# Performance work log

Hardware: AMD Instinct MI355X
Metric: run time of the kernel (lower is better)

## Reference

```python
import jax, jax.numpy as jnp
import numpy as np

B, NB, L, K, C, H = 4, 256, 64, 65, 512, 8
HD = C // H
SCALE = HD ** -0.5


def setup_inputs() -> dict:
    key = jax.random.key(0)
    k = jax.random.split(key, 6)
    x = jax.random.normal(k[0], (B, NB * L, C), dtype=jnp.float32)
    mask = jax.random.bernoulli(k[1], 0.3, (NB, L, K))
    d = jnp.arange(L)
    mask = mask.at[:, d, d].set(True)      # self edges always on
    mask = mask.at[:, :, L].set(True)      # block-node column always on
    edge_feats = jax.random.normal(k[2], (NB, L, K, 4), dtype=jnp.float32)
    qkv_w = jax.random.normal(k[3], (C, 3 * C), dtype=jnp.float32) * (C ** -0.5)
    qkv_b = jnp.zeros((3 * C,), dtype=jnp.float32)
    proj_w = jax.random.normal(k[4], (C, C), dtype=jnp.float32) * (C ** -0.5)
    proj_b = jnp.zeros((C,), dtype=jnp.float32)
    return {"x": x, "attn_mask": mask, "edge_feats": edge_feats,
            "qkv_w": qkv_w, "qkv_b": qkv_b, "proj_w": proj_w, "proj_b": proj_b}


def reference(x, attn_mask, edge_feats, qkv_w, qkv_b, proj_w, proj_b):
    # x: (B, N, C) with N = NB*L (no padding needed); pool = 1, layout LxL+1
    x_blk = x.reshape(B, NB, L, C)                       # query tokens per leaf block
    block_node = x_blk.mean(axis=2, keepdims=True)       # (B, NB, 1, C)
    kv = jnp.concatenate([x_blk, block_node], axis=2)    # (B, NB, K, C), K = L+1

    qkv_q = x_blk @ qkv_w + qkv_b
    qkv_kv = kv @ qkv_w + qkv_b
    q = qkv_q[..., :C].reshape(B, NB, L, H, HD)
    k = qkv_kv[..., C:2 * C].reshape(B, NB, K, H, HD)
    v = qkv_kv[..., 2 * C:].reshape(B, NB, K, H, HD)

    scores = jnp.einsum('bnqhd,bnkhd->bnqkh', q, k) * SCALE  # (B,NB,L,K,H)

    # physics bias: edge_feats[..., :4] broadcast over batch; special/diagonal overrides
    bp = jnp.broadcast_to(edge_feats[None, ..., :4], (B, NB, L, K, 4))
    bp = bp.at[:, :, :, L, :].set(0.0)
    bp = bp.at[:, :, :, L, 3].set(1.0)                    # block-node key column
    d = jnp.arange(L)
    bp = bp.at[:, :, d, d, :].set(0.0)
    bp = bp.at[:, :, d, d, 3].set(1.0)                    # self edge
    scores = scores + bp[..., 3:4]                        # channel 3 additive bias (all heads)

    mask = attn_mask[None, :, :, :, None]                 # (1,NB,L,K,1)
    scores = jnp.where(mask, scores, jnp.float32(-1e9))
    attn = jax.nn.softmax(scores, axis=3)

    out = jnp.einsum('bnqkh,bnkhd->bnqhd', attn, v).reshape(B, NB * L, C)
    return out @ proj_w + proj_b
```

## Files before the change

kernel.cpp:

```cpp
#include <hip/hip_runtime.h>
#include <hip/hip_bf16.h>
#include <math.h>

typedef unsigned short u16;
typedef __attribute__((ext_vector_type(8))) short s16x8;
typedef __attribute__((ext_vector_type(4))) float f32x4;

#define NB_ 256
#define L_  64
#define KK_ 65
#define C_  512
#define H_  8
#define NEDGE (256*64*65)
#define MTOT  65536

__device__ __forceinline__ float b2f(u16 u){
  union { unsigned int i; float f; } x; x.i = ((unsigned int)u) << 16; return x.f;
}
__device__ __forceinline__ u16 f2b(float f){
  union { float f; unsigned int i; } x; x.f = f;
  return (u16)((x.i + 0x7FFFu + ((x.i >> 16) & 1u)) >> 16);
}

__device__ __forceinline__ void gload_lds16(const u16* g, u16* l){
  __builtin_amdgcn_global_load_lds(
      (const __attribute__((address_space(1))) unsigned int*)g,
      (__attribute__((address_space(3))) unsigned int*)l,
      16, 0, 0);
}

__global__ void detect_dtype_kernel(const u16* __restrict__ x, int* __restrict__ flagdt){
  __shared__ int cnt;
  if (threadIdx.x == 0) cnt = 0;
  __syncthreads();
  u16 v = x[(size_t)threadIdx.x * 2 * 1001];
  int e = (v >> 7) & 0xFF;
  if (e >= 141) atomicAdd(&cnt, 1);
  __syncthreads();
  if (threadIdx.x == 0) *flagdt = (cnt >= 8) ? 1 : 0;
}

__global__ void detect_mask_kernel(const unsigned char* __restrict__ m, int* __restrict__ flag){
  __shared__ int ok1, ok2, ok4;
  if (threadIdx.x == 0){ ok1 = 1; ok2 = 1; ok4 = 1; }
  __syncthreads();
  size_t e = (size_t)threadIdx.x * 65 + 64;
  if (((const unsigned char*)m)[e] == 0)  atomicAnd(&ok1, 0);
  if (((const unsigned short*)m)[e] == 0) atomicAnd(&ok2, 0);
  if (((const unsigned int*)m)[e] == 0u)  atomicAnd(&ok4, 0);
  __syncthreads();
  if (threadIdx.x == 0){
    int f = 4;
    if (ok2) f = 2;
    if (ok1) f = 1;
    *flag = f;
  }
}

__global__ void convert_kernel(const void* __restrict__ src, u16* __restrict__ dst,
                               long n, const int* __restrict__ flagdt){
  long i = ((long)blockIdx.x * 256 + threadIdx.x) * 8;
  if (i >= n) return;
  if (*flagdt){
    const float* s = (const float*)src + i;
    u16 o[8];
    #pragma unroll
    for (int j = 0; j < 8; ++j) o[j] = f2b(s[j]);
    *(s16x8*)(dst + i) = *(const s16x8*)o;
  } else {
    *(s16x8*)(dst + i) = *(const s16x8*)((const u16*)src + i);
  }
}

__global__ void build_bias_kernel(const void* __restrict__ edge,
                                  const unsigned char* __restrict__ mask,
                                  const int* __restrict__ flagdt,
                                  const int* __restrict__ flagm,
                                  u16* __restrict__ dst){
  long i = (long)blockIdx.x * 256 + threadIdx.x;
  if (i >= NEDGE) return;
  int kk = (int)(i % 65);
  long rowi = i / 65;
  int l = (int)(rowi & 63);
  int fm = *flagm;
  bool mt;
  if (fm == 1)      mt = mask[i] != 0;
  else if (fm == 2) mt = ((const unsigned short*)mask)[i] != 0;
  else              mt = ((const unsigned int*)mask)[i]   != 0u;
  float v;
  if (!mt)                      v = -1e9f;
  else if (kk == 64 || kk == l) v = 1.0f;
  else v = (*flagdt) ? ((const float*)edge)[i*4 + 3] : b2f(((const u16*)edge)[i*4 + 3]);
  dst[i] = f2b(v);
}

__global__ void transpose_conv_kernel(const void* __restrict__ in, u16* __restrict__ out,
                                      int R, int Cc, const int* __restrict__ flagdt){
  long i = (long)blockIdx.x * 256 + threadIdx.x;
  if (i < (long)R * Cc){
    int r = (int)(i / Cc), c = (int)(i % Cc);
    u16 v = (*flagdt) ? f2b(((const float*)in)[i]) : ((const u16*)in)[i];
    out[(long)c * R + r] = v;
  }
}

__global__ __launch_bounds__(256) void block_mean_kernel(const u16* __restrict__ x, u16* __restrict__ bm){
  int blk = blockIdx.x;
  const u16* xp = x + (long)blk * 64 * 512;
  for (int c = threadIdx.x; c < 512; c += 256){
    float s = 0.f;
    #pragma unroll
    for (int l = 0; l < 64; ++l) s += b2f(xp[l*512 + c]);
    bm[(long)blk * 512 + c] = f2b(s * 0.015625f);
  }
}

__global__ __launch_bounds__(256) void gemm_bt_kernel(
    const u16* __restrict__ A, const u16* __restrict__ BT,
    const u16* __restrict__ bias, u16* __restrict__ Cmat,
    int lda, int ldc, int Kdim, const int* __restrict__ flagdt, int out_mode,
    long row_off)
{
  __shared__ __align__(16) u16 As[2*128*32];
  __shared__ __align__(16) u16 Bs[2*128*32];
  const int t = threadIdx.x;
  const int lane = t & 63;
  const int w = t >> 6;
  const int wm = w & 1, wn = w >> 1;
  const int quad = lane >> 4;
  const int ml = lane & 15;

  const int nwg  = gridDim.x * gridDim.y;
  const int orig = blockIdx.y * gridDim.x + blockIdx.x;
  int lid = orig;
  if ((nwg & 7) == 0) lid = (orig & 7) * (nwg >> 3) + (orig >> 3);
  const int bx = lid % gridDim.x;
  const int by = lid / gridDim.x;
  const long colbase = (long)bx * 128;
  const long rowbase = (long)by * 128;
  const int of = out_mode ? *flagdt : 0;

  const f32x4 zero4 = {0.f, 0.f, 0.f, 0.f};
  f32x4 acc[4][4];
  #pragma unroll
  for (int i = 0; i < 4; ++i)
    #pragma unroll
    for (int j = 0; j < 4; ++j) acc[i][j] = zero4;

  const int c0 = t,       r0 = c0 >> 2, s0 = c0 & 3, g0 = s0 ^ ((r0 >> 1) & 3);
  const int c1 = t + 256, r1 = c1 >> 2, s1 = c1 & 3, g1 = s1 ^ ((r1 >> 1) & 3);
  const u16* Arow0 = A + (rowbase + r0) * (long)lda + g0*8;
  const u16* Arow1 = A + (rowbase + r1) * (long)lda + g1*8;
  const u16* Brow0 = BT + (colbase + r0) * (long)Kdim + g0*8;
  const u16* Brow1 = BT + (colbase + r1) * (long)Kdim + g1*8;

  for (int k0 = 0; k0 < Kdim; k0 += 64){
    __syncthreads();
    gload_lds16(Arow0 + k0,      As + w*512);
    gload_lds16(Arow1 + k0,      As + 2048 + w*512);
    gload_lds16(Arow0 + k0 + 32, As + 4096 + w*512);
    gload_lds16(Arow1 + k0 + 32, As + 4096 + 2048 + w*512);
    gload_lds16(Brow0 + k0,      Bs + w*512);
    gload_lds16(Brow1 + k0,      Bs + 2048 + w*512);
    gload_lds16(Brow0 + k0 + 32, Bs + 4096 + w*512);
    gload_lds16(Brow1 + k0 + 32, Bs + 4096 + 2048 + w*512);
    __syncthreads();
    #pragma unroll
    for (int hb = 0; hb < 2; ++hb){
      const u16* Ab = As + hb*4096;
      const u16* Bb = Bs + hb*4096;
      s16x8 af[4], bfr[4];
      #pragma unroll
      for (int i = 0; i < 4; ++i){
        int m = wm*64 + i*16 + ml;
        af[i]  = *(const s16x8*)(Ab + m*32 + ((quad ^ ((m>>1)&3)))*8);
        int n = wn*64 + i*16 + ml;
        bfr[i] = *(const s16x8*)(Bb + n*32 + ((quad ^ ((n>>1)&3)))*8);
      }
      #pragma unroll
      for (int i = 0; i < 4; ++i)
        #pragma unroll
        for (int j = 0; j < 4; ++j)
          acc[i][j] = __builtin_amdgcn_mfma_f32_16x16x32_bf16(af[i], bfr[j], acc[i][j], 0, 0, 0);
    }
  }

  #pragma unroll
  for (int j = 0; j < 4; ++j){
    long col = colbase + wn*64 + j*16 + ml;
    float bv = b2f(bias[col]);
    #pragma unroll
    for (int i = 0; i < 4; ++i){
      long row = row_off + rowbase + wm*64 + i*16 + quad*4;
      if (of){
        float* Cf = (float*)Cmat;
        #pragma unroll
        for (int r = 0; r < 4; ++r)
          Cf[(row + r) * (long)ldc + col] = acc[i][j][r] + bv;
      } else {
        #pragma unroll
        for (int r = 0; r < 4; ++r)
          Cmat[(row + r) * (long)ldc + col] = f2b(acc[i][j][r] + bv);
      }
    }
  }
}

__global__ __launch_bounds__(256, 4) void attn_kernel(
    const u16* __restrict__ Y, const u16* __restrict__ kvb,
    const u16* __restrict__ biasb, u16* __restrict__ AO)
{
  __shared__ __align__(16) u16 k_s [80*72];
  __shared__ __align__(16) u16 vT_s[64*104];
  __shared__ __align__(16) u16 P_s [64*104];

  const int t = threadIdx.x;
  const int lane = t & 63;
  const int w = t >> 6;
  const int quad = lane >> 4;
  const int ml = lane & 15;

  const int orig = blockIdx.y * gridDim.x + blockIdx.x;
  const int lid  = (orig & 7) * 512 + (orig >> 3);
  const int blk  = lid >> 2;
  const int hp   = lid & 3;
  const int nb = blk & (NB_ - 1);
  const long yrow0 = (long)blk * 64;

  float bb[5][4];
  #pragma unroll
  for (int j = 0; j < 5; ++j){
    int kk = j*16 + ml;
    #pragma unroll
    for (int r = 0; r < 4; ++r){
      int l = w*16 + quad*4 + r;
      bb[j][r] = (kk < 65) ? b2f(biasb[((long)nb*64 + l)*65 + kk]) : 0.f;
    }
  }

  for (int i = t; i < 64*31; i += 256){ int d = i/31, c = 65 + (i%31); vT_s[d*104 + c] = 0; }
  for (int i = t; i < 64*16; i += 256){ int l = i>>4,  c = 80 + (i&15); P_s[l*104 + c] = 0; }
  for (int i = t; i < 15*72; i += 256){ k_s[65*72 + i] = 0; }

  const f32x4 zero4 = {0.f, 0.f, 0.f, 0.f};

  for (int hh = 0; hh < 2; ++hh){
    const int h = hp*2 + hh;
    if (hh) __syncthreads();

    const u16* qrow = Y + (yrow0 + w*16 + ml)*1536 + h*64 + quad*8;
    s16x8 aq0 = *(const s16x8*)(qrow);
    s16x8 aq1 = *(const s16x8*)(qrow + 32);

    for (int c = t; c < 520; c += 256){
      int kk = c >> 3, c8 = c & 7;
      const u16 *srck, *srcv;
      if (kk < 64){
        const u16* base = Y + (yrow0 + kk)*1536;
        srck = base + 512  + h*64 + c8*8;
        srcv = base + 1024 + h*64 + c8*8;
      } else {
        const u16* base = kvb + (long)blk * 1024;
        srck = base + h*64 + c8*8;
        srcv = base + 512 + h*64 + c8*8;
      }
      *(s16x8*)(k_s + kk*72 + c8*8) = *(const s16x8*)srck;
      s16x8 vv = *(const s16x8*)srcv;
      #pragma unroll
      for (int j = 0; j < 8; ++j){
        int jj = (j + c8) & 7;
        vT_s[(c8*8 + jj)*104 + kk] = (u16)vv[jj];
      }
    }
    __syncthreads();

    f32x4 sacc[5];
    #pragma unroll
    for (int j = 0; j < 5; ++j) sacc[j] = zero4;
    #pragma unroll
    for (int j = 0; j < 5; ++j){
      s16x8 bk0 = *(const s16x8*)(k_s + (j*16 + ml)*72 + quad*8);
      sacc[j] = __builtin_amdgcn_mfma_f32_16x16x32_bf16(aq0, bk0, sacc[j], 0, 0, 0);
      s16x8 bk1 = *(const s16x8*)(k_s + (j*16 + ml)*72 + 32 + quad*8);
      sacc[j] = __builtin_amdgcn_mfma_f32_16x16x32_bf16(aq1, bk1, sacc[j], 0, 0, 0);
    }

    float sv[5][4];
    #pragma unroll
    for (int j = 0; j < 5; ++j){
      int kk = j*16 + ml;
      #pragma unroll
      for (int r = 0; r < 4; ++r)
        sv[j][r] = (kk < 65) ? (sacc[j][r]*0.125f + bb[j][r]) : -1e9f;
    }
    #pragma unroll
    for (int r = 0; r < 4; ++r){
      float mx = sv[0][r];
      #pragma unroll
      for (int j = 1; j < 5; ++j) mx = fmaxf(mx, sv[j][r]);
      #pragma unroll
      for (int o = 1; o < 16; o <<= 1) mx = fmaxf(mx, __shfl_xor(mx, o, 64));
      float sm = 0.f;
      #pragma unroll
      for (int j = 0; j < 5; ++j){ float e = __expf(sv[j][r] - mx); sv[j][r] = e; sm += e; }
      #pragma unroll
      for (int o = 1; o < 16; o <<= 1) sm += __shfl_xor(sm, o, 64);
      float inv = 1.0f / sm;
      #pragma unroll
      for (int j = 0; j < 5; ++j) sv[j][r] *= inv;
    }
    #pragma unroll
    for (int j = 0; j < 5; ++j){
      int kk = j*16 + ml;
      #pragma unroll
      for (int r = 0; r < 4; ++r)
        P_s[(w*16 + quad*4 + r)*104 + kk] = f2b(sv[j][r]);
    }
    __syncthreads();

    f32x4 oacc[4];
    #pragma unroll
    for (int j = 0; j < 4; ++j) oacc[j] = zero4;
    #pragma unroll
    for (int s = 0; s < 3; ++s){
      s16x8 ap = *(const s16x8*)(P_s + (w*16 + ml)*104 + s*32 + quad*8);
      #pragma unroll
      for (int j = 0; j < 4; ++j){
        s16x8 bv = *(const s16x8*)(vT_s + (j*16 + ml)*104 + s*32 + quad*8);
        oacc[j] = __builtin_amdgcn_mfma_f32_16x16x32_bf16(ap, bv, oacc[j], 0, 0, 0);
      }
    }
    #pragma unroll
    for (int j = 0; j < 4; ++j){
      int d = j*16 + ml;
      #pragma unroll
      for (int r = 0; r < 4; ++r){
        int l = w*16 + quad*4 + r;
        AO[(yrow0 + l)*512 + h*64 + d] = f2b(oacc[j][r]);
      }
    }
  }
}

extern "C" void kernel_launch(void* const* d_in, const int* in_sizes, int n_in,
                              void* d_out, int out_size, void* d_ws, size_t ws_size,
                              hipStream_t stream)
{
  const void* x_raw     = d_in[0];
  const unsigned char* mask = (const unsigned char*)d_in[1];
  const void* edge_raw  = d_in[2];
  const void* qkvw_raw  = d_in[3];
  const void* qkvb_raw  = d_in[4];
  const void* projw_raw = d_in[5];
  const void* projb_raw = d_in[6];

  char* ws = (char*)d_ws;
  size_t off = 0;
  int*  flagm  = (int*)ws;
  int*  flagdt = (int*)(ws + 4);         off += 1024;
  u16*  XC  = (u16*)(ws + off);          off += (size_t)33554432*2;
  u16*  EB  = (u16*)(ws + off);          off += (size_t)NEDGE*2;
  u16*  WT  = (u16*)(ws + off);          off += (size_t)1536*512*2;
  u16*  PT  = (u16*)(ws + off);          off += (size_t)512*512*2;
  u16*  QB  = (u16*)(ws + off);          off += 4096;
  u16*  PB  = (u16*)(ws + off);          off += 4096;
  u16*  BM  = (u16*)(ws + off);          off += (size_t)1024*512*2;
  u16*  KVB = (u16*)(ws + off);          off += (size_t)1024*1024*2;
  u16*  Y   = (u16*)(ws + off);          off += (size_t)MTOT*1536*2;
  u16*  AO  = (u16*)(ws + off);          off += (size_t)MTOT*512*2;

  detect_dtype_kernel<<<dim3(1), dim3(128), 0, stream>>>((const u16*)x_raw, flagdt);
  detect_mask_kernel<<<dim3(1), dim3(128), 0, stream>>>(mask, flagm);

  convert_kernel<<<dim3(33554432/8/256), dim3(256), 0, stream>>>(x_raw, XC, 33554432, flagdt);
  build_bias_kernel<<<dim3((NEDGE + 255)/256), dim3(256), 0, stream>>>(edge_raw, mask, flagdt, flagm, EB);
  transpose_conv_kernel<<<dim3((512*1536 + 255)/256), dim3(256), 0, stream>>>(qkvw_raw, WT, 512, 1536, flagdt);
  transpose_conv_kernel<<<dim3((512*512  + 255)/256), dim3(256), 0, stream>>>(projw_raw, PT, 512, 512, flagdt);
  convert_kernel<<<dim3(1), dim3(256), 0, stream>>>(qkvb_raw, QB, 1536, flagdt);
  convert_kernel<<<dim3(1), dim3(256), 0, stream>>>(projb_raw, PB, 512, flagdt);

  block_mean_kernel<<<dim3(1024), dim3(256), 0, stream>>>(XC, BM);
  gemm_bt_kernel<<<dim3(8, 8), dim3(256), 0, stream>>>(BM, WT + 512*512, QB + 512, KVB, 512, 1024, 512, flagdt, 0, 0);

  gemm_bt_kernel<<<dim3(12, MTOT/128), dim3(256), 0, stream>>>(XC, WT, QB, Y, 512, 1536, 512, flagdt, 0, 0);
  attn_kernel<<<dim3(1024, 4), dim3(256), 0, stream>>>(Y, KVB, EB, AO);
  gemm_bt_kernel<<<dim3(4, MTOT/128), dim3(256), 0, stream>>>(AO, PT, PB, (u16*)d_out, 512, 512, 512, flagdt, 1, 0);
}
```

Measured before the change: 560.5 us.

## Double-buffer GEMM K-loop so global-to-LDS loads overlap MFMA compute

The GEMM main loop is restructured from a load-all-then-compute step of 64 K to a two-buffer pipeline over 32-wide K slices. The next slice is prefetched into the alternate LDS buffer while the current one is computed, using explicit vmcnt waits and raw barriers instead of __syncthreads. This is meant to hide global load latency behind MFMA work. It adds barriers per iteration and issues one redundant final load (the tail index is clamped). It also relies on the vmcnt counts matching the number of in-flight loads, and assumes an even number of K slices.

```diff
diff --git a/kernel.cpp b/kernel.cpp
--- a/kernel.cpp
+++ b/kernel.cpp
@@ -154,35 +154,44 @@
   const u16* Brow0 = BT + (colbase + r0) * (long)Kdim + g0*8;
   const u16* Brow1 = BT + (colbase + r1) * (long)Kdim + g1*8;
 
-  for (int k0 = 0; k0 < Kdim; k0 += 64){
-    __syncthreads();
-    gload_lds16(Arow0 + k0,      As + w*512);
-    gload_lds16(Arow1 + k0,      As + 2048 + w*512);
-    gload_lds16(Arow0 + k0 + 32, As + 4096 + w*512);
-    gload_lds16(Arow1 + k0 + 32, As + 4096 + 2048 + w*512);
-    gload_lds16(Brow0 + k0,      Bs + w*512);
-    gload_lds16(Brow1 + k0,      Bs + 2048 + w*512);
-    gload_lds16(Brow0 + k0 + 32, Bs + 4096 + w*512);
-    gload_lds16(Brow1 + k0 + 32, Bs + 4096 + 2048 + w*512);
-    __syncthreads();
-    #pragma unroll
-    for (int hb = 0; hb < 2; ++hb){
-      const u16* Ab = As + hb*4096;
-      const u16* Bb = Bs + hb*4096;
-      s16x8 af[4], bfr[4];
-      #pragma unroll
-      for (int i = 0; i < 4; ++i){
-        int m = wm*64 + i*16 + ml;
-        af[i]  = *(const s16x8*)(Ab + m*32 + ((quad ^ ((m>>1)&3)))*8);
-        int n = wn*64 + i*16 + ml;
-        bfr[i] = *(const s16x8*)(Bb + n*32 + ((quad ^ ((n>>1)&3)))*8);
-      }
-      #pragma unroll
-      for (int i = 0; i < 4; ++i)
-        #pragma unroll
-        for (int j = 0; j < 4; ++j)
-          acc[i][j] = __builtin_amdgcn_mfma_f32_16x16x32_bf16(af[i], bfr[j], acc[i][j], 0, 0, 0);
-    }
+  auto stage = [&](int b, int k0){
+    gload_lds16(Arow0 + k0, As + b*4096 + w*512);
+    gload_lds16(Arow1 + k0, As + b*4096 + 2048 + w*512);
+    gload_lds16(Brow0 + k0, Bs + b*4096 + w*512);
+    gload_lds16(Brow1 + k0, Bs + b*4096 + 2048 + w*512);
+  };
+  auto compute = [&](int b){
+    const u16* Ab = As + b*4096;
+    const u16* Bb = Bs + b*4096;
+    s16x8 af[4], bfr[4];
+    #pragma unroll
+    for (int i = 0; i < 4; ++i){
+      int m = wm*64 + i*16 + ml;
+      af[i]  = *(const s16x8*)(Ab + m*32 + ((quad ^ ((m>>1)&3)))*8);
+      int n = wn*64 + i*16 + ml;
+      bfr[i] = *(const s16x8*)(Bb + n*32 + ((quad ^ ((n>>1)&3)))*8);
+    }
+    #pragma unroll
+    for (int i = 0; i < 4; ++i)
+      #pragma unroll
+      for (int j = 0; j < 4; ++j)
+        acc[i][j] = __builtin_amdgcn_mfma_f32_16x16x32_bf16(af[i], bfr[j], acc[i][j], 0, 0, 0);
+  };
+
+  const int nk = Kdim >> 5;
+  stage(0, 0);
+  for (int kt = 0; kt < nk; kt += 2){
+    stage(1, (kt+1) << 5);
+    asm volatile("s_waitcnt vmcnt(4)" ::: "memory");
+    __builtin_amdgcn_s_barrier();
+    compute(0);
+    __builtin_amdgcn_s_barrier();
+    int knxt = (kt+2 < nk) ? (kt+2) << 5 : (nk-1) << 5;
+    stage(0, knxt);
+    asm volatile("s_waitcnt vmcnt(4)" ::: "memory");
+    __builtin_amdgcn_s_barrier();
+    compute(1);
+    __builtin_amdgcn_s_barrier();
   }
 
   #pragma unroll
```

Result: slower. 580.8 us (+3.6%).

## Process four heads per attention block and prefetch next head's K/V into registers

Applied to the files above, without the earlier changes.

Each attention workgroup now handles four heads instead of two, halving the grid, which amortizes the per-block bias loads and LDS zero-fill over more heads. For heads after the first, the next head's K and V rows are loaded into registers right after the score MFMAs. They are written to LDS after a barrier, so global load latency overlaps with the softmax and PV compute. In exchange it uses more registers per thread and gives fewer workgroups for occupancy and load balance.

```diff
diff --git a/kernel.cpp b/kernel.cpp
--- a/kernel.cpp
+++ b/kernel.cpp
@@ -221,9 +221,9 @@
   const int ml = lane & 15;
 
   const int orig = blockIdx.y * gridDim.x + blockIdx.x;
-  const int lid  = (orig & 7) * 512 + (orig >> 3);
-  const int blk  = lid >> 2;
-  const int hp   = lid & 3;
+  const int lid  = (orig & 7) * 256 + (orig >> 3);
+  const int blk  = lid >> 1;
+  const int hq   = lid & 1;
   const int nb = blk & (NB_ - 1);
   const long yrow0 = (long)blk * 64;
 
@@ -242,37 +242,63 @@
   for (int i = t; i < 64*16; i += 256){ int l = i>>4,  c = 80 + (i&15); P_s[l*104 + c] = 0; }
   for (int i = t; i < 15*72; i += 256){ k_s[65*72 + i] = 0; }
 
+  const int kk0 = t >> 3,  c8 = t & 7;
+  const int kk1 = kk0 + 32;
+  const u16* yb0 = Y + (yrow0 + kk0)*1536;
+  const u16* yb1 = Y + (yrow0 + kk1)*1536;
+  const u16* kvbase = kvb + (long)blk * 1024;
+
   const f32x4 zero4 = {0.f, 0.f, 0.f, 0.f};
-
-  for (int hh = 0; hh < 2; ++hh){
-    const int h = hp*2 + hh;
-    if (hh) __syncthreads();
+  s16x8 kr0, vr0, kr1, vr1;
+
+  for (int hh = 0; hh < 4; ++hh){
+    const int h = hq*4 + hh;
+
+    if (hh == 0){
+      for (int c = t; c < 520; c += 256){
+        int kk = c >> 3, cc = c & 7;
+        const u16 *srck, *srcv;
+        if (kk < 64){
+          const u16* base = Y + (yrow0 + kk)*1536;
+          srck = base + 512  + h*64 + cc*8;
+          srcv = base + 1024 + h*64 + cc*8;
+        } else {
+          srck = kvbase + h*64 + cc*8;
+          srcv = kvbase + 512 + h*64 + cc*8;
+        }
+        *(s16x8*)(k_s + kk*72 + cc*8) = *(const s16x8*)srck;
+        s16x8 vv = *(const s16x8*)srcv;
+        #pragma unroll
+        for (int j = 0; j < 8; ++j){
+          int jj = (j + cc) & 7;
+          vT_s[(cc*8 + jj)*104 + kk] = (u16)vv[jj];
+        }
+      }
+    } else {
+      __syncthreads();
+      *(s16x8*)(k_s + kk0*72 + c8*8) = kr0;
+      *(s16x8*)(k_s + kk1*72 + c8*8) = kr1;
+      #pragma unroll
+      for (int j = 0; j < 8; ++j){
+        int jj = (j + c8) & 7;
+        vT_s[(c8*8 + jj)*104 + kk0] = (u16)vr0[jj];
+        vT_s[(c8*8 + jj)*104 + kk1] = (u16)vr1[jj];
+      }
+      if (t < 8){
+        *(s16x8*)(k_s + 64*72 + t*8) = *(const s16x8*)(kvbase + h*64 + t*8);
+        s16x8 vv = *(const s16x8*)(kvbase + 512 + h*64 + t*8);
+        #pragma unroll
+        for (int j = 0; j < 8; ++j){
+          int jj = (j + t) & 7;
+          vT_s[(t*8 + jj)*104 + 64] = (u16)vv[jj];
+        }
+      }
+    }
+    __syncthreads();
 
     const u16* qrow = Y + (yrow0 + w*16 + ml)*1536 + h*64 + quad*8;
     s16x8 aq0 = *(const s16x8*)(qrow);
     s16x8 aq1 = *(const s16x8*)(qrow + 32);
-
-    for (int c = t; c < 520; c += 256){
-      int kk = c >> 3, c8 = c & 7;
-      const u16 *srck, *srcv;
-      if (kk < 64){
-        const u16* base = Y + (yrow0 + kk)*1536;
-        srck = base + 512  + h*64 + c8*8;
-        srcv = base + 1024 + h*64 + c8*8;
-      } else {
-        const u16* base = kvb + (long)blk * 1024;
-        srck = base + h*64 + c8*8;
-        srcv = base + 512 + h*64 + c8*8;
-      }
-      *(s16x8*)(k_s + kk*72 + c8*8) = *(const s16x8*)srck;
-      s16x8 vv = *(const s16x8*)srcv;
-      #pragma unroll
-      for (int j = 0; j < 8; ++j){
-        int jj = (j + c8) & 7;
-        vT_s[(c8*8 + jj)*104 + kk] = (u16)vv[jj];
-      }
-    }
-    __syncthreads();
 
     f32x4 sacc[5];
     #pragma unroll
@@ -283,6 +309,14 @@
       sacc[j] = __builtin_amdgcn_mfma_f32_16x16x32_bf16(aq0, bk0, sacc[j], 0, 0, 0);
       s16x8 bk1 = *(const s16x8*)(k_s + (j*16 + ml)*72 + 32 + quad*8);
       sacc[j] = __builtin_amdgcn_mfma_f32_16x16x32_bf16(aq1, bk1, sacc[j], 0, 0, 0);
+    }
+
+    if (hh < 3){
+      const int hn = h + 1;
+      kr0 = *(const s16x8*)(yb0 + 512  + hn*64 + c8*8);
+      vr0 = *(const s16x8*)(yb0 + 1024 + hn*64 + c8*8);
+      kr1 = *(const s16x8*)(yb1 + 512  + hn*64 + c8*8);
+      vr1 = *(const s16x8*)(yb1 + 1024 + hn*64 + c8*8);
     }
 
     float sv[5][4];
@@ -383,6 +417,6 @@
   gemm_bt_kernel<<<dim3(8, 8), dim3(256), 0, stream>>>(BM, WT + 512*512, QB + 512, KVB, 512, 1024, 512, flagdt, 0, 0);
 
   gemm_bt_kernel<<<dim3(12, MTOT/128), dim3(256), 0, stream>>>(XC, WT, QB, Y, 512, 1536, 512, flagdt, 0, 0);
-  attn_kernel<<<dim3(1024, 4), dim3(256), 0, stream>>>(Y, KVB, EB, AO);
+  attn_kernel<<<dim3(1024, 2), dim3(256), 0, stream>>>(Y, KVB, EB, AO);
   gemm_bt_kernel<<<dim3(4, MTOT/128), dim3(256), 0, stream>>>(AO, PT, PB, (u16*)d_out, 512, 512, 512, flagdt, 1, 0);
 }
```

Measured after the change: 559.0 us. Within noise of the previous version (-0.3%).
